# Optimization experiments

Measured on AMD Instinct MI355X. Metric: run time of the kernel, lower is better.

Reference implementation:

```python
import jax, jax.numpy as jnp
import numpy as np

B, L, T = 4, 512, 4096
HID, NH = 1024, 16
HD = HID // NH
MAX_POS = 4096
BASE = 10000.0


def _cos_sin(dim, max_pos, base):
    inv_freq = 1.0 / base ** (jnp.arange(0, dim, 2, dtype=jnp.float32) / dim)
    t = jnp.arange(max_pos, dtype=jnp.float32)
    freqs = jnp.einsum('i,j->ij', t, inv_freq)
    emb = jnp.concatenate([freqs, freqs], axis=-1)  # [max_pos, dim]
    return jnp.cos(emb), jnp.sin(emb)


def _rotate_half(x):
    x1, x2 = x[..., : x.shape[-1] // 2], x[..., x.shape[-1] // 2:]
    return jnp.concatenate([-x2, x1], axis=-1)


def setup_inputs() -> dict:
    key = jax.random.key(0)
    ks = jax.random.split(key, 12)
    s = 0.02
    inp = {
        'latents': jax.random.normal(ks[0], (B, L, HID), jnp.float32),
        'target': jax.random.normal(ks[1], (B, T, HID), jnp.float32),
        'target_mask': jax.random.randint(ks[2], (B, T), 0, 2).astype(bool),
        'target_timestamp': jnp.sort(jax.random.randint(ks[3], (B, T), 0, MAX_POS), axis=-1),
        'Wq': jax.random.normal(ks[4], (HID, HID), jnp.float32) * s,
        'bq': jnp.zeros((HID,), jnp.float32),
        'Wk': jax.random.normal(ks[5], (HID, HID), jnp.float32) * s,
        'bk': jnp.zeros((HID,), jnp.float32),
        'Wv': jax.random.normal(ks[6], (HID, HID), jnp.float32) * s,
        'bv': jnp.zeros((HID,), jnp.float32),
        'Wo': jax.random.normal(ks[7], (HID, HID), jnp.float32) * s,
        'bo': jnp.zeros((HID,), jnp.float32),
    }
    return inp


def reference(latents, target, target_mask, target_timestamp, Wq, bq, Wk, bk, Wv, bv, Wo, bo):
    cos, sin = _cos_sin(HD, MAX_POS, BASE)  # [MAX_POS, HD]
    # latents_timestamp: arange(L) * (max-1)/(L-1), cast to int
    lat_ts = (jnp.arange(L, dtype=jnp.float32) * (MAX_POS - 1) / (L - 1)).astype(jnp.int64)
    lat_ts = jnp.broadcast_to(lat_ts[None, :], (B, L))

    # QKV projections (torch Linear: x @ W.T + b)
    q = (latents @ Wq.T + bq).reshape(B, L, NH, HD).transpose(0, 2, 1, 3)  # [B,H,L,D]
    k = (target @ Wk.T + bk).reshape(B, T, NH, HD).transpose(0, 2, 1, 3)   # [B,H,T,D]
    v = (target @ Wv.T + bv).reshape(B, T, NH, HD).transpose(0, 2, 1, 3)

    # RoPE with gathered timestamps; unsqueeze over head dim
    cq, sq = cos[lat_ts][:, None], sin[lat_ts][:, None]          # [B,1,L,D]
    ck, sk = cos[target_timestamp][:, None], sin[target_timestamp][:, None]  # [B,1,T,D]
    q = q * cq + _rotate_half(q) * sq
    k = k * ck + _rotate_half(k) * sk

    # SDPA with boolean attn mask (True = attend)
    scores = jnp.einsum('bhld,bhtd->bhlt', q, k) / jnp.sqrt(jnp.float32(HD))
    bias = jnp.where(target_mask[:, None, None, :], 0.0, -jnp.inf).astype(scores.dtype)
    attn = jax.nn.softmax(scores + bias, axis=-1)
    out = jnp.einsum('bhlt,bhtd->bhld', attn, v)  # [B,H,L,D]
    out = out.transpose(0, 2, 1, 3).reshape(B, L, HID)
    return out @ Wo.T + bo
```

## Files before the change

kernel.cpp:

```cpp
#include <hip/hip_runtime.h>

#define B_ 4
#define L_ 512
#define T_ 4096
#define NH_ 16
#define HD_ 64

using f32x4 = __attribute__((ext_vector_type(4))) float;
using bf16x8 = __attribute__((ext_vector_type(8))) short;
using u32x4 = __attribute__((ext_vector_type(4))) unsigned int;

__device__ __forceinline__ unsigned short f2bf(float x) {
  unsigned int u = __builtin_bit_cast(unsigned int, x);
  u += 0x7fffu + ((u >> 16) & 1u);
  return (unsigned short)(u >> 16);
}

__device__ __forceinline__ unsigned cvtpk(float lo, float hi) {
  unsigned r;
  asm("v_cvt_pk_bf16_f32 %0, %1, %2" : "=v"(r) : "v"(lo), "v"(hi));
  return r;
}

__device__ __forceinline__ u32x4 cvt8(const float4& a, const float4& b) {
  u32x4 r;
  r[0] = (unsigned)f2bf(a.x) | ((unsigned)f2bf(a.y) << 16);
  r[1] = (unsigned)f2bf(a.z) | ((unsigned)f2bf(a.w) << 16);
  r[2] = (unsigned)f2bf(b.x) | ((unsigned)f2bf(b.y) << 16);
  r[3] = (unsigned)f2bf(b.z) | ((unsigned)f2bf(b.w) << 16);
  return r;
}

__device__ __forceinline__ void gload16(const void* g, void* l) {
  __builtin_amdgcn_global_load_lds(
      (const __attribute__((address_space(1))) unsigned int*)g,
      (__attribute__((address_space(3))) unsigned int*)l, 16, 0, 0);
}

#define BC8(x) __builtin_bit_cast(bf16x8, (x))

struct CvtArgs {
  const float* src[6];
  unsigned short* dst[6];
  int cum[7];
};

__global__ void cvt_bf16(CvtArgs a, int total) {
  for (int g = blockIdx.x * 256 + threadIdx.x; g < total; g += gridDim.x * 256) {
    int r = 0;
#pragma unroll
    for (int q = 0; q < 5; ++q) r += (g >= a.cum[q + 1]);
    const int lc = g - a.cum[r];
    const float4* s = (const float4*)a.src[r] + (size_t)lc * 2;
    float4 x0 = s[0], x1 = s[1];
    *((u32x4*)a.dst[r] + lc) = cvt8(x0, x1);
  }
}

__global__ void rope_table(float* __restrict__ cost, float* __restrict__ sint,
                           const int* __restrict__ mask, float* __restrict__ mbias) {
  const int idx = blockIdx.x * 256 + threadIdx.x;
  const int pos = idx >> 5, i = idx & 31;
  const float inv = 1.0f / powf(10000.0f, (float)(2 * i) * (1.0f / 64.0f));
  const float f = (float)pos * inv;
  cost[idx] = cosf(f);
  sint[idx] = sinf(f);
  if (idx < B_ * T_) mbias[idx] = mask[idx] ? 0.f : -1e30f;
}

template <int EPI>
__global__ __launch_bounds__(256, 2) void gemm_bf(
    const unsigned short* __restrict__ A, const unsigned short* __restrict__ Wb,
    const float* __restrict__ bias, void* __restrict__ outp,
    const float* __restrict__ cost, const float* __restrict__ sint,
    const int* __restrict__ ts) {
  __shared__ u32x4 lsA[2][512];
  __shared__ u32x4 lsB[2][512];
  const int tid = threadIdx.x;
  const int mt = blockIdx.x >> 3, nt = blockIdx.x & 7;
  const int mBase = mt << 7, nBase = nt << 7;
  const int lane = tid & 63, wid = tid >> 6;
  const int wr = wid >> 1, wc = wid & 1;
  const int lr = lane & 15, lg = lane >> 4;

  f32x4 acc[4][4];
#pragma unroll
  for (int m = 0; m < 4; ++m)
#pragma unroll
    for (int n = 0; n < 4; ++n) acc[m][n] = (f32x4){0.f, 0.f, 0.f, 0.f};

  auto stage = [&](int bi, int kt) {
    const int ko = kt * 32;
#pragma unroll
    for (int j2 = 0; j2 < 2; ++j2) {
      const int j = wid * 2 + j2;
      const int row = (j & 1) * 64 + lane;
      const int kg = j >> 1;
      gload16(A + (size_t)(mBase + row) * 1024 + ko + kg * 8,
              (unsigned short*)lsA[bi] + j * 512);
      gload16(Wb + (size_t)(nBase + row) * 1024 + ko + kg * 8,
              (unsigned short*)lsB[bi] + j * 512);
    }
  };

  stage(0, 0);
  __syncthreads();
  int cur = 0;
  for (int kt = 0; kt < 32; ++kt) {
    if (kt < 31) stage(cur ^ 1, kt + 1);
    const u32x4* As = lsA[cur];
    const u32x4* Bs = lsB[cur];
    bf16x8 af[4], bfr[4];
#pragma unroll
    for (int m = 0; m < 4; ++m) af[m] = BC8(As[lg * 128 + wr * 64 + m * 16 + lr]);
#pragma unroll
    for (int n = 0; n < 4; ++n) bfr[n] = BC8(Bs[lg * 128 + wc * 64 + n * 16 + lr]);
#pragma unroll
    for (int m = 0; m < 4; ++m)
#pragma unroll
      for (int n = 0; n < 4; ++n)
        acc[m][n] = __builtin_amdgcn_mfma_f32_16x16x32_bf16(af[m], bfr[n], acc[m][n], 0, 0, 0);
    __syncthreads();
    cur ^= 1;
  }

  float bv[4];
#pragma unroll
  for (int n = 0; n < 4; ++n) bv[n] = bias[nBase + wc * 64 + n * 16 + lr];

  if (EPI == 3) {
    float* Of = (float*)outp;
#pragma unroll
    for (int m = 0; m < 4; ++m)
#pragma unroll
      for (int r = 0; r < 4; ++r) {
        const int gR = mBase + wr * 64 + m * 16 + lg * 4 + r;
#pragma unroll
        for (int n = 0; n < 4; ++n)
          Of[(size_t)gR * 1024 + nBase + wc * 64 + n * 16 + lr] = acc[m][n][r] + bv[n];
      }
  } else {
    unsigned short* Qo = (unsigned short*)outp;
    const int h = (nBase >> 6) + wc;
#pragma unroll
    for (int m = 0; m < 4; ++m) {
#pragma unroll
      for (int r = 0; r < 4; ++r) {
        const int gR = mBase + wr * 64 + m * 16 + lg * 4 + r;
        const int b2 = gR >> 9, p2 = gR & 511;
        const int pos = (int)(((float)p2 * 4095.0f) / 511.0f);
        const float* cp = cost + pos * 32;
        const float* sp = sint + pos * 32;
        const size_t obase = (((size_t)(b2 * NH_ + h)) * L_ + p2) * HD_;
#pragma unroll
        for (int n = 0; n < 2; ++n) {
          const int d = n * 16 + lr;
          const float x1 = acc[m][n][r] + bv[n];
          const float x2 = acc[m][n + 2][r] + bv[n + 2];
          const float c = cp[d], s = sp[d];
          Qo[obase + d] = f2bf(x1 * c - x2 * s);
          Qo[obase + d + 32] = f2bf(x2 * c + x1 * s);
        }
      }
    }
  }
}

__global__ __launch_bounds__(512, 1) void gemm_kv8(
    const unsigned short* __restrict__ A, const unsigned short* __restrict__ Wkv,
    const float* __restrict__ bkp, const float* __restrict__ bvp,
    unsigned short* __restrict__ Ko, unsigned short* __restrict__ Vo,
    const float* __restrict__ cost, const float* __restrict__ sint,
    const int* __restrict__ ts) {
  __shared__ u32x4 lds_[8192];
  const int tid = threadIdx.x;
  const int lane = tid & 63, w = tid >> 6;
  const int wm = w >> 2, wn = w & 3;
  const int lr = lane & 15, lg = lane >> 4;
  const int orig = blockIdx.x;
  const int wgid = (orig & 7) * 64 + (orig >> 3);
  const int mt = wgid >> 3, nt = wgid & 7;
  const int mBase = mt << 8, nBase = nt << 8;

  f32x4 acc[8][4];
#pragma unroll
  for (int m = 0; m < 8; ++m)
#pragma unroll
    for (int n = 0; n < 4; ++n) acc[m][n] = (f32x4){0.f, 0.f, 0.f, 0.f};

  auto stage = [&](int kt1, int q) {
    char* ab = (char*)lds_ + (kt1 & 1) * 65536 + q * 16384;
#pragma unroll
    for (int c = 0; c < 2; ++c) {
      const int g0 = c * 512 + w * 64;
      const int row = (g0 & 255) + lane;
      const int kc = q * 4 + (g0 >> 8);
      const size_t koff = (size_t)(kt1 * 64 + kc * 8);
      gload16(A + (size_t)(mBase + row) * 1024 + koff, ab + g0 * 16);
      gload16(Wkv + (size_t)(nBase + row) * 1024 + koff, ab + 32768 + g0 * 16);
    }
  };

  stage(0, 0);
  stage(0, 1);

  for (int kt = 0; kt < 16; ++kt) {
    const u32x4* Ab = lds_ + (kt & 1) * 4096;
    const u32x4* Bb = Ab + 2048;
#pragma unroll
    for (int q = 0; q < 2; ++q) {
      if (kt == 15 && q == 1)
        asm volatile("s_waitcnt vmcnt(0)" ::: "memory");
      else
        asm volatile("s_waitcnt vmcnt(4)" ::: "memory");
      __builtin_amdgcn_s_barrier();
      const int kidx = q * 4 + lg;
      bf16x8 af[8], bfq[4];
#pragma unroll
      for (int m = 0; m < 8; ++m)
        af[m] = BC8(Ab[kidx * 256 + wm * 128 + m * 16 + lr]);
#pragma unroll
      for (int n = 0; n < 4; ++n)
        bfq[n] = BC8(Bb[kidx * 256 + wn * 64 + n * 16 + lr]);
      if (kt < 15) stage(kt + 1, q);
      asm volatile("s_waitcnt lgkmcnt(0)" ::: "memory");
      __builtin_amdgcn_sched_barrier(0);
      __builtin_amdgcn_s_setprio(1);
#pragma unroll
      for (int m = 0; m < 8; ++m)
#pragma unroll
        for (int n = 0; n < 4; ++n)
          acc[m][n] = __builtin_amdgcn_mfma_f32_16x16x32_bf16(af[m], bfq[n], acc[m][n], 0, 0, 0);
      __builtin_amdgcn_s_setprio(0);
    }
  }

  const bool isV = (nt >= 4);
  const float* bp = isV ? bvp : bkp;
  const int h = (nt & 3) * 4 + wn;
  float bb[4];
#pragma unroll
  for (int n = 0; n < 4; ++n) bb[n] = bp[(nt & 3) * 256 + wn * 64 + n * 16 + lr];

  if (!isV) {
#pragma unroll
    for (int m = 0; m < 8; ++m) {
#pragma unroll
      for (int r = 0; r < 4; ++r) {
        const int gR = mBase + wm * 128 + m * 16 + lg * 4 + r;
        const int b2 = gR >> 12, p2 = gR & 4095;
        const int pos = ts[gR];
        const float* cp = cost + pos * 32;
        const float* sp = sint + pos * 32;
        const size_t obase = (((size_t)(b2 * NH_ + h)) * T_ + p2) * HD_;
#pragma unroll
        for (int n = 0; n < 2; ++n) {
          const int d = n * 16 + lr;
          const float x1 = acc[m][n][r] + bb[n];
          const float x2 = acc[m][n + 2][r] + bb[n + 2];
          const float c = cp[d], s = sp[d];
          Ko[obase + d] = f2bf(x1 * c - x2 * s);
          Ko[obase + d + 32] = f2bf(x2 * c + x1 * s);
        }
      }
    }
  } else {
#pragma unroll
    for (int m = 0; m < 8; ++m) {
      const int r0 = mBase + wm * 128 + m * 16 + lg * 4;
      const int b = r0 >> 12, t = r0 & 4095;
#pragma unroll
      for (int n = 0; n < 4; ++n) {
        const int d = n * 16 + lr;
        ushort4 pk;
        pk.x = f2bf(acc[m][n][0] + bb[n]);
        pk.y = f2bf(acc[m][n][1] + bb[n]);
        pk.z = f2bf(acc[m][n][2] + bb[n]);
        pk.w = f2bf(acc[m][n][3] + bb[n]);
        *(ushort4*)(Vo + (((size_t)(b * NH_ + h)) * HD_ + d) * (size_t)T_ + t) = pk;
      }
    }
  }
}

#define SCL 0.180336880111f
__global__ __launch_bounds__(256, 4) void attn_half(
    const unsigned short* __restrict__ Q, const unsigned short* __restrict__ K,
    const unsigned short* __restrict__ V, const float* __restrict__ mbias,
    float* __restrict__ pws, float* __restrict__ mlws) {
  __shared__ u32x4 QP[512];
  __shared__ u32x4 Ks[2][512];
  __shared__ u32x4 Vs[2][512];
  const int tid = threadIdx.x, lane = tid & 63, w = tid >> 6;
  const int lr = lane & 15, lg = lane >> 4;
  const int orig = blockIdx.x;
  const int wg = (orig & 7) * 128 + (orig >> 3);
  const int half = wg & 1, lt = (wg >> 1) & 7, bh = wg >> 4;
  const int b = bh >> 4;
  const int l0 = lt << 6;
  const int tBase = half << 11;

#pragma unroll
  for (int i = 0; i < 2; ++i) {
    const int li = w * 2 + i;
    gload16(Q + ((size_t)bh * L_ + l0 + lane) * HD_ + li * 8, (unsigned short*)QP + li * 512);
  }
  __syncthreads();
  bf16x8 qf[2];
#pragma unroll
  for (int ks2 = 0; ks2 < 2; ++ks2)
    qf[ks2] = BC8(QP[(ks2 * 4 + lg) * 64 + w * 16 + lr]);

  f32x4 po[4];
#pragma unroll
  for (int n = 0; n < 4; ++n) po[n] = (f32x4){0.f, 0.f, 0.f, 0.f};
  float mrun = -1e30f, lrun = 0.f;

  char* Pw = (char*)QP + w * 2048;
  const int swz = (lr & 7) << 4;
  const float* mrow = mbias + (size_t)b * T_ + tBase;

  auto stage = [&](int bi, int it) {
    const int t0 = tBase + (it << 6);
#pragma unroll
    for (int i = 0; i < 2; ++i) {
      const int li = w * 2 + i;
      gload16(K + ((size_t)bh * T_ + t0 + lane) * HD_ + li * 8, (unsigned short*)Ks[bi] + li * 512);
      gload16(V + ((size_t)bh * HD_ + lane) * T_ + t0 + li * 8, (unsigned short*)Vs[bi] + li * 512);
    }
  };

  stage(0, 0);
  __syncthreads();
  int cur = 0;
  for (int it = 0; it < 32; ++it) {
    if (it < 31) stage(cur ^ 1, it + 1);
    const int t0l = it << 6;

    f32x4 s[4];
#pragma unroll
    for (int n = 0; n < 4; ++n) s[n] = (f32x4){0.f, 0.f, 0.f, 0.f};
#pragma unroll
    for (int ks2 = 0; ks2 < 2; ++ks2) {
#pragma unroll
      for (int n = 0; n < 4; ++n) {
        bf16x8 kb = BC8(Ks[cur][(ks2 * 4 + lg) * 64 + n * 16 + lr]);
        s[n] = __builtin_amdgcn_mfma_f32_16x16x32_bf16(kb, qf[ks2], s[n], 0, 0, 0);
      }
    }
#pragma unroll
    for (int n = 0; n < 4; ++n) {
      const f32x4 mb = *(const f32x4*)(mrow + t0l + n * 16 + lg * 4);
#pragma unroll
      for (int r = 0; r < 4; ++r) s[n][r] = s[n][r] * SCL + mb[r];
    }
    f32x4 m4;
#pragma unroll
    for (int r = 0; r < 4; ++r)
      m4[r] = fmaxf(fmaxf(s[0][r], s[1][r]), fmaxf(s[2][r], s[3][r]));
    float x = fmaxf(fmaxf(m4[0], m4[1]), fmaxf(m4[2], m4[3]));
    x = fmaxf(x, __shfl_xor(x, 16));
    x = fmaxf(x, __shfl_xor(x, 32));
    const float mnew = fmaxf(mrun, x);
    const float sc = __builtin_exp2f(mrun - mnew);
    mrun = mnew;
    f32x4 ls4 = (f32x4){0.f, 0.f, 0.f, 0.f};
#pragma unroll
    for (int n = 0; n < 4; ++n)
#pragma unroll
      for (int r = 0; r < 4; ++r) {
        const float p = __builtin_exp2f(s[n][r] - mnew);
        s[n][r] = p;
        ls4[r] += p;
      }
    lrun = lrun * sc + ((ls4[0] + ls4[1]) + (ls4[2] + ls4[3]));
#pragma unroll
    for (int n = 0; n < 4; ++n) po[n] *= sc;
#pragma unroll
    for (int n = 0; n < 4; ++n) {
      uint2 pk;
      pk.x = cvtpk(s[n][0], s[n][1]);
      pk.y = cvtpk(s[n][2], s[n][3]);
      *(uint2*)(Pw + ((lr * 128 + n * 32 + lg * 8) ^ swz)) = pk;
    }
    bf16x8 pa[2];
#pragma unroll
    for (int ks2 = 0; ks2 < 2; ++ks2)
      pa[ks2] = BC8(*(const u32x4*)(Pw + ((lr * 128 + ks2 * 64 + lg * 16) ^ swz)));
#pragma unroll
    for (int ks2 = 0; ks2 < 2; ++ks2) {
#pragma unroll
      for (int n = 0; n < 4; ++n) {
        bf16x8 vb = BC8(Vs[cur][(ks2 * 4 + lg) * 64 + n * 16 + lr]);
        po[n] = __builtin_amdgcn_mfma_f32_16x16x32_bf16(vb, pa[ks2], po[n], 0, 0, 0);
      }
    }
    __syncthreads();
    cur ^= 1;
  }

  lrun += __shfl_xor(lrun, 16);
  lrun += __shfl_xor(lrun, 32);
  const int l = w * 16 + lr;
  float* pbase = pws + ((size_t)(((bh << 3) + lt) * 2 + half)) * 4096;
  float* mlbase = mlws + ((size_t)(((bh << 3) + lt) * 2 + half)) * 128;
#pragma unroll
  for (int n = 0; n < 4; ++n)
    *(f32x4*)(pbase + l * 64 + n * 16 + lg * 4) = po[n];
  if (lg == 0) {
    mlbase[l * 2] = mrun;
    mlbase[l * 2 + 1] = lrun;
  }
}

__global__ void attn_combine(const float* __restrict__ pws, const float* __restrict__ mlws,
                             unsigned short* __restrict__ O) {
  const int blk = blockIdx.x;
  const int bh = blk >> 3, lt = blk & 7;
  const int b = bh >> 4, h = bh & 15;
  const int tid = threadIdx.x;
  const int row = tid >> 2, seg = tid & 3;
  const float* p0 = pws + ((size_t)blk * 2) * 4096 + row * 64 + seg * 16;
  const float* p1 = p0 + 4096;
  const float* ml0 = mlws + ((size_t)blk * 2) * 128 + row * 2;
  const float* ml1 = ml0 + 128;
  const float m0 = ml0[0], li0 = ml0[1], m1 = ml1[0], li1 = ml1[1];
  const float M = fmaxf(m0, m1);
  const float w0 = __builtin_exp2f(m0 - M), w1 = __builtin_exp2f(m1 - M);
  const float inv = 1.0f / (li0 * w0 + li1 * w1);
  const int gl = lt * 64 + row;
  unsigned short* orow = O + ((size_t)b * L_ + gl) * 1024 + h * HD_ + seg * 16;
#pragma unroll
  for (int j = 0; j < 4; ++j) {
    const float4 a = *(const float4*)(p0 + j * 4);
    const float4 c = *(const float4*)(p1 + j * 4);
    ushort4 pk;
    pk.x = f2bf((a.x * w0 + c.x * w1) * inv);
    pk.y = f2bf((a.y * w0 + c.y * w1) * inv);
    pk.z = f2bf((a.z * w0 + c.z * w1) * inv);
    pk.w = f2bf((a.w * w0 + c.w * w1) * inv);
    *(ushort4*)(orow + j * 4) = pk;
  }
}

extern "C" void kernel_launch(void* const* d_in, const int* in_sizes, int n_in,
                              void* d_out, int out_size, void* d_ws, size_t ws_size,
                              hipStream_t stream) {
  const float* latents = (const float*)d_in[0];
  const float* target = (const float*)d_in[1];
  const int* mask = (const int*)d_in[2];
  const int* ts = (const int*)d_in[3];
  const float* Wq = (const float*)d_in[4];
  const float* bq = (const float*)d_in[5];
  const float* Wk = (const float*)d_in[6];
  const float* bk = (const float*)d_in[7];
  const float* Wv = (const float*)d_in[8];
  const float* bv = (const float*)d_in[9];
  const float* Wo = (const float*)d_in[10];
  const float* bo = (const float*)d_in[11];
  float* out = (float*)d_out;

  char* ws = (char*)d_ws;
  float* cost = (float*)ws;
  float* sint = (float*)(ws + (512 << 10));
  unsigned short* Qws = (unsigned short*)(ws + (1ull << 20));
  unsigned short* Kws = (unsigned short*)(ws + (5ull << 20));
  unsigned short* Vws = (unsigned short*)(ws + (37ull << 20));
  float* mbias = (float*)(ws + (69ull << 20));
  unsigned short* Ows = (unsigned short*)(ws + (69ull << 20));
  unsigned short* latb = (unsigned short*)(ws + (73ull << 20));
  unsigned short* tgtb = (unsigned short*)(ws + (77ull << 20));
  float* pws = (float*)(ws + (77ull << 20));
  float* mlws = (float*)(ws + (93ull << 20));
  unsigned short* Wqb = (unsigned short*)(ws + (109ull << 20));
  unsigned short* Wkvb = (unsigned short*)(ws + (111ull << 20));
  unsigned short* Wob = (unsigned short*)(ws + (115ull << 20));

  CvtArgs ca;
  ca.src[0] = latents; ca.dst[0] = latb;
  ca.src[1] = target;  ca.dst[1] = tgtb;
  ca.src[2] = Wq;      ca.dst[2] = Wqb;
  ca.src[3] = Wk;      ca.dst[3] = Wkvb;
  ca.src[4] = Wv;      ca.dst[4] = Wkvb + (1 << 20);
  ca.src[5] = Wo;      ca.dst[5] = Wob;
  const int nch[6] = {2097152 / 8, 16777216 / 8, 131072, 131072, 131072, 131072};
  ca.cum[0] = 0;
  for (int i = 0; i < 6; ++i) ca.cum[i + 1] = ca.cum[i] + nch[i];
  const int total = ca.cum[6];

  cvt_bf16<<<dim3(2048), dim3(256), 0, stream>>>(ca, total);
  rope_table<<<dim3(512), dim3(256), 0, stream>>>(cost, sint, mask, mbias);
  gemm_bf<0><<<dim3(16 * 8), dim3(256), 0, stream>>>(latb, Wqb, bq, Qws, cost, sint, nullptr);
  gemm_kv8<<<dim3(512), dim3(512), 0, stream>>>(tgtb, Wkvb, bk, bv, Kws, Vws, cost, sint, ts);
  attn_half<<<dim3(1024), dim3(256), 0, stream>>>(Qws, Kws, Vws, mbias, pws, mlws);
  attn_combine<<<dim3(512), dim3(256), 0, stream>>>(pws, mlws, Ows);
  gemm_bf<3><<<dim3(16 * 8), dim3(256), 0, stream>>>(Ows, Wob, bo, out, nullptr, nullptr, nullptr);
}
```

Measured before the change: 327.2 us.

## Prefetch two K-tiles ahead in KV projection GEMM and split fragment loads

```diff
diff --git a/kernel.cpp b/kernel.cpp
--- a/kernel.cpp
+++ b/kernel.cpp
@@ -188,51 +188,64 @@
 #pragma unroll
     for (int n = 0; n < 4; ++n) acc[m][n] = (f32x4){0.f, 0.f, 0.f, 0.f};
 
-  auto stage = [&](int kt1, int q) {
-    char* ab = (char*)lds_ + (kt1 & 1) * 65536 + q * 16384;
-#pragma unroll
-    for (int c = 0; c < 2; ++c) {
+  auto stage = [&](int kt1) {
+    char* ab = (char*)lds_ + (kt1 & 1) * 65536;
+#pragma unroll
+    for (int c = 0; c < 4; ++c) {
       const int g0 = c * 512 + w * 64;
       const int row = (g0 & 255) + lane;
-      const int kc = q * 4 + (g0 >> 8);
+      const int kc = g0 >> 8;
       const size_t koff = (size_t)(kt1 * 64 + kc * 8);
       gload16(A + (size_t)(mBase + row) * 1024 + koff, ab + g0 * 16);
       gload16(Wkv + (size_t)(nBase + row) * 1024 + koff, ab + 32768 + g0 * 16);
     }
   };
 
-  stage(0, 0);
-  stage(0, 1);
+  stage(0);
+  stage(1);
 
   for (int kt = 0; kt < 16; ++kt) {
     const u32x4* Ab = lds_ + (kt & 1) * 4096;
     const u32x4* Bb = Ab + 2048;
-#pragma unroll
-    for (int q = 0; q < 2; ++q) {
-      if (kt == 15 && q == 1)
-        asm volatile("s_waitcnt vmcnt(0)" ::: "memory");
-      else
-        asm volatile("s_waitcnt vmcnt(4)" ::: "memory");
-      __builtin_amdgcn_s_barrier();
-      const int kidx = q * 4 + lg;
-      bf16x8 af[8], bfq[4];
-#pragma unroll
-      for (int m = 0; m < 8; ++m)
-        af[m] = BC8(Ab[kidx * 256 + wm * 128 + m * 16 + lr]);
-#pragma unroll
-      for (int n = 0; n < 4; ++n)
-        bfq[n] = BC8(Bb[kidx * 256 + wn * 64 + n * 16 + lr]);
-      if (kt < 15) stage(kt + 1, q);
+    if (kt == 15)
+      asm volatile("s_waitcnt vmcnt(0)" ::: "memory");
+    else
+      asm volatile("s_waitcnt vmcnt(8)" ::: "memory");
+    __builtin_amdgcn_s_barrier();
+
+#pragma unroll
+    for (int kk = 0; kk < 2; ++kk) {
+      const int kidx = kk * 4 + lg;
+      bf16x8 af[4], bfq[4];
+#pragma unroll
+      for (int n = 0; n < 4; ++n) bfq[n] = BC8(Bb[kidx * 256 + wn * 64 + n * 16 + lr]);
+#pragma unroll
+      for (int m = 0; m < 4; ++m) af[m] = BC8(Ab[kidx * 256 + wm * 128 + m * 16 + lr]);
       asm volatile("s_waitcnt lgkmcnt(0)" ::: "memory");
       __builtin_amdgcn_sched_barrier(0);
       __builtin_amdgcn_s_setprio(1);
 #pragma unroll
-      for (int m = 0; m < 8; ++m)
+      for (int m = 0; m < 4; ++m)
 #pragma unroll
         for (int n = 0; n < 4; ++n)
           acc[m][n] = __builtin_amdgcn_mfma_f32_16x16x32_bf16(af[m], bfq[n], acc[m][n], 0, 0, 0);
       __builtin_amdgcn_s_setprio(0);
-    }
+#pragma unroll
+      for (int m = 0; m < 4; ++m)
+        af[m] = BC8(Ab[kidx * 256 + wm * 128 + (m + 4) * 16 + lr]);
+      asm volatile("s_waitcnt lgkmcnt(0)" ::: "memory");
+      __builtin_amdgcn_sched_barrier(0);
+      __builtin_amdgcn_s_setprio(1);
+#pragma unroll
+      for (int m = 0; m < 4; ++m)
+#pragma unroll
+        for (int n = 0; n < 4; ++n)
+          acc[m + 4][n] = __builtin_amdgcn_mfma_f32_16x16x32_bf16(af[m], bfq[n], acc[m + 4][n], 0, 0, 0);
+      __builtin_amdgcn_s_setprio(0);
+    }
+
+    __builtin_amdgcn_s_barrier();
+    if (kt < 14) stage(kt + 2);
   }
 
   const bool isV = (nt >= 4);
```

New measurement: 320.6 us. 2.0% less time.
